# Optimization experiments

Measured on AMD Instinct MI355X. Metric: run time of the kernel, lower is better.

The kernel has to match this reference:

```python
import jax, jax.numpy as jnp
import numpy as np


def setup_inputs() -> dict:
    key = jax.random.key(0)
    k1, k2 = jax.random.split(key)
    n_tokens, embed_dim, num_embed = 16384, 512, 2048
    encode = jax.random.normal(k1, (n_tokens, embed_dim), dtype=jnp.float32)
    # Embedding init in torch: uniform(-1/num_embed, 1/num_embed)
    templat = jax.random.uniform(
        k2, (num_embed, embed_dim), dtype=jnp.float32,
        minval=-1.0 / num_embed, maxval=1.0 / num_embed)
    return {"encode": encode, "templat": templat}


def reference(encode, templat):
    # match_encode_with_templat, eval path: sample=False, detach='encode', metric='l2'
    encode_d = jax.lax.stop_gradient(encode)
    # squared L2 distance: ||e||^2 - 2 e@t^T + ||t||^2 ; logits = -dist
    e_sq = jnp.sum(encode_d * encode_d, axis=-1, keepdims=True)       # (N, 1)
    t_sq = jnp.sum(templat * templat, axis=-1)[None, :]               # (1, M)
    dist = e_sq - 2.0 * (encode_d @ templat.T) + t_sq                 # (N, M)
    logits = -dist
    zsoft = jax.nn.softmax(logits, axis=-1)
    zidx = jnp.argmax(zsoft, axis=-1)                                 # (N,)
    quant = templat[zidx]                                             # (N, C) gather
    return quant, zidx
```

## Files before the change

kernel.cpp:

```cpp
#include <hip/hip_runtime.h>
#include <stdint.h>

#define N_TOK  16384
#define EMB    512
#define NEMB   2048
#define NCHUNK 32
#define CWIN   2.5e-4f
#define WCAP   524288

typedef __attribute__((ext_vector_type(8))) short s16x8;
typedef __attribute__((ext_vector_type(4))) float f32x4;

__device__ __forceinline__ unsigned short f2bf(float f) {
  unsigned u = __float_as_uint(f);
  u += 0x7fffu + ((u >> 16) & 1u);
  return (unsigned short)(u >> 16);
}
__device__ __forceinline__ unsigned mapf(float f) {
  unsigned u = __float_as_uint(f);
  return (u >> 31) ? ~u : (u | 0x80000000u);
}
__device__ __forceinline__ float unmapf(unsigned u) {
  return __uint_as_float((u >> 31) ? (u & 0x7fffffffu) : ~u);
}

__device__ __forceinline__ float pairwise512_sq(const float* se, int lane) {
  int l = lane & 31;
  int b = l >> 3, j = l & 7;
  const float* base = se + b * 128 + j;
  float x = base[0];
  float r = __fmul_rn(x, x);
#pragma unroll
  for (int k = 1; k < 16; ++k) {
    float y = base[8 * k];
    r = __fadd_rn(r, __fmul_rn(y, y));
  }
  r = __fadd_rn(r, __shfl_xor(r, 1));
  r = __fadd_rn(r, __shfl_xor(r, 2));
  r = __fadd_rn(r, __shfl_xor(r, 4));
  r = __fadd_rn(r, __shfl_xor(r, 8));
  r = __fadd_rn(r, __shfl_xor(r, 16));
  return r;
}

__global__ __launch_bounds__(256) void prep_kernel(
    const float* __restrict__ tmp, const float* __restrict__ enc,
    unsigned short* __restrict__ thi, float* __restrict__ tsq,
    unsigned short* __restrict__ ehi, float* __restrict__ esq,
    int* __restrict__ wcount) {
  __shared__ float se[4][EMB];
  int wv = threadIdx.x >> 6, lane = threadIdx.x & 63;
  int row = blockIdx.x * 4 + wv;
  if (blockIdx.x == 0 && threadIdx.x == 0) *wcount = 0;
  bool isT = row < NEMB;
  const float* src = isT ? (tmp + (size_t)row * EMB)
                         : (enc + (size_t)(row - NEMB) * EMB);
  const float4* p = (const float4*)src + lane * 2;
  float4 v0 = p[0], v1 = p[1];
  float f[8] = {v0.x, v0.y, v0.z, v0.w, v1.x, v1.y, v1.z, v1.w};
  unsigned h[8];
#pragma unroll
  for (int i = 0; i < 8; ++i) { h[i] = f2bf(f[i]); se[wv][lane * 8 + i] = f[i]; }
  uint4 packed = { h[0] | (h[1] << 16), h[2] | (h[3] << 16),
                   h[4] | (h[5] << 16), h[6] | (h[7] << 16) };
  unsigned short* dsth = isT ? (thi + (size_t)row * EMB)
                             : (ehi + (size_t)(row - NEMB) * EMB);
  ((uint4*)dsth)[lane] = packed;
  __syncthreads();
  float s = pairwise512_sq(se[wv], lane);
  if (lane == 0) { if (isT) tsq[row] = s; else esq[row - NEMB] = s; }
}

__global__ __launch_bounds__(512, 2) void score_kernel(
    const unsigned short* __restrict__ ehi, const unsigned short* __restrict__ thi,
    const float* __restrict__ tsq,
    unsigned long long* __restrict__ keyc, unsigned* __restrict__ s2c) {
  __shared__ __align__(16) char smem[131072];
  const int tid = threadIdx.x, w = tid >> 6, lane = tid & 63;
  const int q = lane >> 4, r = lane & 15;
  const int wr = w >> 2, wc = w & 3;
  const int tokb = (int)blockIdx.x >> 3;
  const int nb   = (int)blockIdx.x & 7;

  const int c0 = tid, c1 = 512 + tid;
  const int L0 = (c0 * 16) ^ ((((c0 * 16) >> 9) & 1) << 5);
  const int L1 = (c1 * 16) ^ ((((c1 * 16) >> 9) & 1) << 5);
  const int row0 = L0 >> 6, ce0 = (L0 & 63) >> 1;
  const int row1 = L1 >> 6, ce1 = (L1 & 63) >> 1;
  const unsigned short* pa0 = ehi + (size_t)(tokb * 256 + row0) * EMB + ce0;
  const unsigned short* pa1 = ehi + (size_t)(tokb * 256 + row1) * EMB + ce1;
  const unsigned short* pb0 = thi + (size_t)(nb  * 256 + row0) * EMB + ce0;
  const unsigned short* pb1 = thi + (size_t)(nb  * 256 + row1) * EMB + ce1;

#define STAGE_A(ktp, kk) do {                                                     \
    char* lb_ = smem + ((((ktp) & 1) * 2 + (kk)) << 14) + (w << 10);              \
    __builtin_amdgcn_global_load_lds(                                             \
        (const __attribute__((address_space(1))) void*)(pa0 + (ktp) * 64 + (kk) * 32), \
        (__attribute__((address_space(3))) void*)lb_, 16, 0, 0);                  \
    __builtin_amdgcn_global_load_lds(                                             \
        (const __attribute__((address_space(1))) void*)(pa1 + (ktp) * 64 + (kk) * 32), \
        (__attribute__((address_space(3))) void*)(lb_ + 8192), 16, 0, 0);         \
  } while (0)
#define STAGE_B(ktp, kk) do {                                                     \
    char* lb_ = smem + 65536 + ((((ktp) & 1) * 2 + (kk)) << 14) + (w << 10);      \
    __builtin_amdgcn_global_load_lds(                                             \
        (const __attribute__((address_space(1))) void*)(pb0 + (ktp) * 64 + (kk) * 32), \
        (__attribute__((address_space(3))) void*)lb_, 16, 0, 0);                  \
    __builtin_amdgcn_global_load_lds(                                             \
        (const __attribute__((address_space(1))) void*)(pb1 + (ktp) * 64 + (kk) * 32), \
        (__attribute__((address_space(3))) void*)(lb_ + 8192), 16, 0, 0);         \
  } while (0)

  int offA[8], offB[4];
#pragma unroll
  for (int m = 0; m < 8; ++m) {
    int P = (wr * 128 + m * 16 + r) * 64 + q * 16;
    offA[m] = P ^ (((P >> 9) & 1) << 5);
  }
#pragma unroll
  for (int n = 0; n < 4; ++n) {
    int P = (wc * 64 + n * 16 + r) * 64 + q * 16;
    offB[n] = P ^ (((P >> 9) & 1) << 5);
  }

  f32x4 acc[8][4];
#pragma unroll
  for (int m = 0; m < 8; ++m)
#pragma unroll
    for (int n = 0; n < 4; ++n) acc[m][n] = (f32x4){0.f, 0.f, 0.f, 0.f};

  STAGE_A(0, 0); STAGE_B(0, 0); STAGE_A(0, 1); STAGE_B(0, 1); STAGE_A(1, 0); STAGE_B(1, 0);
  asm volatile("s_waitcnt vmcnt(8)" ::: "memory");
  __builtin_amdgcn_s_barrier();

#define LOADA(kkbase, mh)                                        \
    a0 = *(const s16x8*)(Ab_ + (kkbase) + offA[(mh) * 4 + 0]);   \
    a1 = *(const s16x8*)(Ab_ + (kkbase) + offA[(mh) * 4 + 1]);   \
    a2 = *(const s16x8*)(Ab_ + (kkbase) + offA[(mh) * 4 + 2]);   \
    a3 = *(const s16x8*)(Ab_ + (kkbase) + offA[(mh) * 4 + 3]);
#define LOADB(kkbase)                                            \
    bf4[0] = *(const s16x8*)(Bb_ + (kkbase) + offB[0]);          \
    bf4[1] = *(const s16x8*)(Bb_ + (kkbase) + offB[1]);          \
    bf4[2] = *(const s16x8*)(Bb_ + (kkbase) + offB[2]);          \
    bf4[3] = *(const s16x8*)(Bb_ + (kkbase) + offB[3]);
#define MFMA_HALF(mh)                                                              \
    __builtin_amdgcn_s_setprio(1);                                                 \
    _Pragma("unroll")                                                              \
    for (int n = 0; n < 4; ++n) {                                                  \
      acc[(mh) * 4 + 0][n] = __builtin_amdgcn_mfma_f32_16x16x32_bf16(a0, bf4[n], acc[(mh) * 4 + 0][n], 0, 0, 0); \
      acc[(mh) * 4 + 1][n] = __builtin_amdgcn_mfma_f32_16x16x32_bf16(a1, bf4[n], acc[(mh) * 4 + 1][n], 0, 0, 0); \
      acc[(mh) * 4 + 2][n] = __builtin_amdgcn_mfma_f32_16x16x32_bf16(a2, bf4[n], acc[(mh) * 4 + 2][n], 0, 0, 0); \
      acc[(mh) * 4 + 3][n] = __builtin_amdgcn_mfma_f32_16x16x32_bf16(a3, bf4[n], acc[(mh) * 4 + 3][n], 0, 0, 0); \
    }                                                                              \
    __builtin_amdgcn_s_setprio(0);

#pragma unroll
  for (int kt = 0; kt < 8; ++kt) {
    char* Ab_ = smem + ((kt & 1) * 2 << 14);
    char* Bb_ = smem + 65536 + ((kt & 1) * 2 << 14);
    s16x8 a0, a1, a2, a3, bf4[4];
    LOADA(0, 0); LOADB(0);
    if (kt + 1 < 8) STAGE_A(kt + 1, 1);
    __builtin_amdgcn_s_barrier();
    MFMA_HALF(0);
    __builtin_amdgcn_s_barrier();
    LOADA(0, 1);
    if (kt + 1 < 8) STAGE_B(kt + 1, 1);
    __builtin_amdgcn_s_barrier();
    MFMA_HALF(1);
    if (kt < 7) { asm volatile("s_waitcnt vmcnt(8)" ::: "memory"); }
    else        { asm volatile("s_waitcnt vmcnt(0)" ::: "memory"); }
    __builtin_amdgcn_s_barrier();
    LOADA(16384, 0); LOADB(16384);
    if (kt + 2 < 8) STAGE_A(kt + 2, 0);
    __builtin_amdgcn_s_barrier();
    MFMA_HALF(0);
    __builtin_amdgcn_s_barrier();
    LOADA(16384, 1);
    if (kt + 2 < 8) STAGE_B(kt + 2, 0);
    __builtin_amdgcn_s_barrier();
    MFMA_HALF(1);
    if (kt < 6)       { asm volatile("s_waitcnt vmcnt(8)" ::: "memory"); }
    else if (kt == 6) { asm volatile("s_waitcnt vmcnt(4)" ::: "memory"); }
    __builtin_amdgcn_s_barrier();
  }

  const int chunk = nb * 4 + wc;
  const int nbase = nb * 256 + wc * 64;
  float tq[4];
#pragma unroll
  for (int n = 0; n < 4; ++n) tq[n] = tsq[nbase + n * 16 + r];
#pragma unroll
  for (int m = 0; m < 8; ++m) {
#pragma unroll
    for (int i = 0; i < 4; ++i) {
      unsigned long long k1 = ~0ULL; unsigned s2m = 0xffffffffu;
#pragma unroll
      for (int n = 0; n < 4; ++n) {
        float s = tq[n] - 2.0f * acc[m][n][i];
        unsigned sm = mapf(s);
        unsigned long long k =
            ((unsigned long long)sm << 32) | (unsigned)(nbase + n * 16 + r);
        if (k < k1) { unsigned o = (unsigned)(k1 >> 32); s2m = o < s2m ? o : s2m; k1 = k; }
        else s2m = sm < s2m ? sm : s2m;
      }
#pragma unroll
      for (int mask = 1; mask < 16; mask <<= 1) {
        unsigned long long ok = __shfl_xor(k1, mask);
        unsigned os = __shfl_xor(s2m, mask);
        if (ok < k1) { unsigned o = (unsigned)(k1 >> 32); s2m = o < s2m ? o : s2m; k1 = ok; }
        else { unsigned o = (unsigned)(ok >> 32); s2m = o < s2m ? o : s2m; }
        s2m = os < s2m ? os : s2m;
      }
      if (r == 0) {
        int token = tokb * 256 + wr * 128 + m * 16 + q * 4 + i;
        keyc[(size_t)chunk * N_TOK + token] = k1;
        s2c [(size_t)chunk * N_TOK + token] = s2m;
      }
    }
  }
#undef STAGE_A
#undef STAGE_B
#undef LOADA
#undef LOADB
#undef MFMA_HALF
}

__global__ __launch_bounds__(64) void merge_kernel(
    const unsigned long long* __restrict__ keyc, const unsigned* __restrict__ s2c,
    int* __restrict__ bestIdx, int* __restrict__ flag, int* __restrict__ work,
    int* __restrict__ wcount, unsigned long long* __restrict__ rkey) {
  int t = blockIdx.x * 64 + threadIdx.x;
  if (t >= N_TOK) return;
  rkey[t] = ~0ULL;
  unsigned long long K = ~0ULL; unsigned S = 0xffffffffu;
  for (int c = 0; c < NCHUNK; ++c) {
    unsigned long long k = keyc[(size_t)c * N_TOK + t];
    unsigned s2 = s2c[(size_t)c * N_TOK + t];
    if (k < K) { unsigned o = (unsigned)(K >> 32); S = o < S ? o : S; K = k; }
    else { unsigned o = (unsigned)(k >> 32); S = o < S ? o : S; }
    S = s2 < S ? s2 : S;
  }
  float best_f   = unmapf((unsigned)(K >> 32));
  float second_f = unmapf(S);
  int idx = (int)(unsigned)(K & 0xffffffffu);
  bestIdx[t] = idx;
  bool ok = (second_f - best_f >= CWIN) && (idx >= 0) && (idx < NEMB) && (best_f == best_f);
  flag[t] = ok ? 0 : 1;
  if (!ok) {
    bool nanCase = !(best_f == best_f);
    float limit = best_f + CWIN;
    for (int c = 0; c < NCHUNK; ++c) {
      float cf = unmapf((unsigned)(keyc[(size_t)c * N_TOK + t] >> 32));
      if (nanCase || !(cf > limit)) {
        int pos = atomicAdd(wcount, 1);
        if (pos < WCAP) work[pos] = t * NCHUNK + c;
      }
    }
  }
}

__global__ __launch_bounds__(256) void refine_kernel(
    const float* __restrict__ enc, const float* __restrict__ tmp,
    const float* __restrict__ esq, const float* __restrict__ tsq,
    const int* __restrict__ work, const int* __restrict__ wcount,
    unsigned long long* __restrict__ rkey) {
  int total = *wcount; if (total > WCAP) total = WCAP;
  __shared__ float se[EMB];
  const int wv = threadIdx.x >> 6, lane = threadIdx.x & 63;
  for (int p = blockIdx.x; p < total; p += gridDim.x) {
    __syncthreads();
    int item = work[p];
    int token = item / NCHUNK, c = item % NCHUNK;
    const float4* erow = (const float4*)(enc + (size_t)token * EMB);
    for (int i = threadIdx.x; i < 128; i += 256) ((float4*)se)[i] = erow[i];
    __syncthreads();
    float e2 = esq[token];
    unsigned long long lkey = ~0ULL;
#pragma unroll
    for (int j = 0; j < 16; ++j) {
      int m = c * 64 + wv + j * 4;
      const float4* trow = (const float4*)(tmp + (size_t)m * EMB);
      float4 a0 = trow[lane], a1 = trow[lane + 64];
      float4 b0 = ((const float4*)se)[lane], b1 = ((const float4*)se)[lane + 64];
      double s = (double)a0.x * b0.x + (double)a0.y * b0.y
               + (double)a0.z * b0.z + (double)a0.w * b0.w
               + (double)a1.x * b1.x + (double)a1.y * b1.y
               + (double)a1.z * b1.z + (double)a1.w * b1.w;
#pragma unroll
      for (int mask = 1; mask < 64; mask <<= 1) s += __shfl_xor(s, mask);
      if (lane == 0) {
        float M  = (float)s;
        float d1 = __fadd_rn(e2, -__fmul_rn(2.0f, M));
        float d2 = __fadd_rn(d1, tsq[m]);
        unsigned long long key =
            ((unsigned long long)__float_as_uint(d2) << 32) | (unsigned)m;
        if (key < lkey) lkey = key;
      }
    }
    if (lane == 0 && lkey != ~0ULL) atomicMin(&rkey[token], lkey);
  }
}

__global__ void gather_kernel(const float* __restrict__ tmp, const int* __restrict__ bestIdx,
                              const int* __restrict__ flag,
                              const unsigned long long* __restrict__ rkey,
                              float* __restrict__ out) {
  int token = blockIdx.x * 4 + (threadIdx.x >> 6);
  int lane = threadIdx.x & 63;
  int idx = flag[token] ? (int)(unsigned)(rkey[token] & 0xffffffffULL) : bestIdx[token];
  idx = idx < 0 ? 0 : (idx > NEMB - 1 ? NEMB - 1 : idx);
  const float4* src = (const float4*)(tmp + (size_t)idx * EMB) + lane * 2;
  float4* dst = (float4*)(out + (size_t)token * EMB) + lane * 2;
  dst[0] = src[0];
  dst[1] = src[1];
  if (lane == 0) out[(size_t)N_TOK * EMB + token] = (float)idx;
}

extern "C" void kernel_launch(void* const* d_in, const int* in_sizes, int n_in,
                              void* d_out, int out_size, void* d_ws, size_t ws_size,
                              hipStream_t stream) {
  const float* enc = (const float*)d_in[0];
  const float* tmp = (const float*)d_in[1];
  float* out = (float*)d_out;
  char* ws = (char*)d_ws;
  unsigned short* thi = (unsigned short*)ws;
  unsigned short* ehi = (unsigned short*)(ws + 2097152);
  float* tsq      = (float*)(ws + 18874368);
  float* esq      = (float*)(ws + 18882560);
  unsigned long long* keyc = (unsigned long long*)(ws + 18948096);
  unsigned* s2c   = (unsigned*)(ws + 23142400);
  int*   bestIdx  = (int*)  (ws + 25239552);
  int*   flag     = (int*)  (ws + 25305088);
  unsigned long long* rkey = (unsigned long long*)(ws + 25370624);
  int*   wcount   = (int*)  (ws + 25501696);
  int*   work     = (int*)  (ws + 25501760);

  prep_kernel  <<<4608,      256, 0, stream>>>(tmp, enc, thi, tsq, ehi, esq, wcount);
  score_kernel <<<512,       512, 0, stream>>>(ehi, thi, tsq, keyc, s2c);
  merge_kernel <<<N_TOK/64,  64,  0, stream>>>(keyc, s2c, bestIdx, flag, work, wcount, rkey);
  refine_kernel<<<1024,      256, 0, stream>>>(enc, tmp, esq, tsq, work, wcount, rkey);
  gather_kernel<<<N_TOK/4,   256, 0, stream>>>(tmp, bestIdx, flag, rkey, out);
}
```

Baseline: 209.3 us.

## Process two codebook tiles per score block and use DPP reductions in epilogue

Each score block now computes two 256-wide codebook tiles in sequence and reuses its token tile. The grid drops to 256 blocks with a swizzled block-to-tile mapping, and the next tile's loads are issued before the current epilogue runs. The epilogue's 64-bit key shuffle reduction is replaced by float min and second-min folding over DPP lane swaps, followed by an index recovery pass and vectorized stores. The refine kernel gives each 16-lane group one codebook row instead of having a whole wave reduce over 64 lanes, and the merge kernel uses larger blocks. Running half as many blocks may lower occupancy and CU coverage on a 256-CU device.

```diff
diff --git a/kernel.cpp b/kernel.cpp
--- a/kernel.cpp
+++ b/kernel.cpp
@@ -22,6 +22,16 @@
 }
 __device__ __forceinline__ float unmapf(unsigned u) {
   return __uint_as_float((u >> 31) ? (u & 0x7fffffffu) : ~u);
+}
+
+template<int CTRL>
+__device__ __forceinline__ float dppf(float x) {
+  return __uint_as_float((unsigned)__builtin_amdgcn_update_dpp(
+      0, (int)__float_as_uint(x), CTRL, 0xF, 0xF, true));
+}
+template<int CTRL>
+__device__ __forceinline__ unsigned dppu(unsigned x) {
+  return (unsigned)__builtin_amdgcn_update_dpp(0, (int)x, CTRL, 0xF, 0xF, true);
 }
 
 __device__ __forceinline__ float pairwise512_sq(const float* se, int lane) {
@@ -79,8 +89,10 @@
   const int tid = threadIdx.x, w = tid >> 6, lane = tid & 63;
   const int q = lane >> 4, r = lane & 15;
   const int wr = w >> 2, wc = w & 3;
-  const int tokb = (int)blockIdx.x >> 3;
-  const int nb   = (int)blockIdx.x & 7;
+  const int bid = (int)blockIdx.x;
+  const int sw = (bid & 7) * 32 + (bid >> 3);
+  const int tokb = sw >> 2;
+  const int nbq  = sw & 3;
 
   const int c0 = tid, c1 = 512 + tid;
   const int L0 = (c0 * 16) ^ ((((c0 * 16) >> 9) & 1) << 5);
@@ -89,8 +101,8 @@
   const int row1 = L1 >> 6, ce1 = (L1 & 63) >> 1;
   const unsigned short* pa0 = ehi + (size_t)(tokb * 256 + row0) * EMB + ce0;
   const unsigned short* pa1 = ehi + (size_t)(tokb * 256 + row1) * EMB + ce1;
-  const unsigned short* pb0 = thi + (size_t)(nb  * 256 + row0) * EMB + ce0;
-  const unsigned short* pb1 = thi + (size_t)(nb  * 256 + row1) * EMB + ce1;
+  const unsigned short* pb0 = thi + (size_t)(nbq * 512 + row0) * EMB + ce0;
+  const unsigned short* pb1 = thi + (size_t)(nbq * 512 + row1) * EMB + ce1;
 
 #define STAGE_A(ktp, kk) do {                                                     \
     char* lb_ = smem + ((((ktp) & 1) * 2 + (kk)) << 14) + (w << 10);              \
@@ -122,16 +134,6 @@
     int P = (wc * 64 + n * 16 + r) * 64 + q * 16;
     offB[n] = P ^ (((P >> 9) & 1) << 5);
   }
-
-  f32x4 acc[8][4];
-#pragma unroll
-  for (int m = 0; m < 8; ++m)
-#pragma unroll
-    for (int n = 0; n < 4; ++n) acc[m][n] = (f32x4){0.f, 0.f, 0.f, 0.f};
-
-  STAGE_A(0, 0); STAGE_B(0, 0); STAGE_A(0, 1); STAGE_B(0, 1); STAGE_A(1, 0); STAGE_B(1, 0);
-  asm volatile("s_waitcnt vmcnt(8)" ::: "memory");
-  __builtin_amdgcn_s_barrier();
 
 #define LOADA(kkbase, mh)                                        \
     a0 = *(const s16x8*)(Ab_ + (kkbase) + offA[(mh) * 4 + 0]);   \
@@ -154,69 +156,100 @@
     }                                                                              \
     __builtin_amdgcn_s_setprio(0);
 
-#pragma unroll
-  for (int kt = 0; kt < 8; ++kt) {
-    char* Ab_ = smem + ((kt & 1) * 2 << 14);
-    char* Bb_ = smem + 65536 + ((kt & 1) * 2 << 14);
-    s16x8 a0, a1, a2, a3, bf4[4];
-    LOADA(0, 0); LOADB(0);
-    if (kt + 1 < 8) STAGE_A(kt + 1, 1);
+  f32x4 acc[8][4];
+
+  STAGE_A(0, 0); STAGE_B(0, 0); STAGE_A(0, 1); STAGE_B(0, 1); STAGE_A(1, 0); STAGE_B(1, 0);
+
+#pragma unroll 1
+  for (int half = 0; half < 2; ++half) {
+    if (half == 0) { asm volatile("s_waitcnt vmcnt(8)" ::: "memory"); }
+    else           { asm volatile("s_waitcnt vmcnt(0)" ::: "memory"); }
     __builtin_amdgcn_s_barrier();
-    MFMA_HALF(0);
-    __builtin_amdgcn_s_barrier();
-    LOADA(0, 1);
-    if (kt + 1 < 8) STAGE_B(kt + 1, 1);
-    __builtin_amdgcn_s_barrier();
-    MFMA_HALF(1);
-    if (kt < 7) { asm volatile("s_waitcnt vmcnt(8)" ::: "memory"); }
-    else        { asm volatile("s_waitcnt vmcnt(0)" ::: "memory"); }
-    __builtin_amdgcn_s_barrier();
-    LOADA(16384, 0); LOADB(16384);
-    if (kt + 2 < 8) STAGE_A(kt + 2, 0);
-    __builtin_amdgcn_s_barrier();
-    MFMA_HALF(0);
-    __builtin_amdgcn_s_barrier();
-    LOADA(16384, 1);
-    if (kt + 2 < 8) STAGE_B(kt + 2, 0);
-    __builtin_amdgcn_s_barrier();
-    MFMA_HALF(1);
-    if (kt < 6)       { asm volatile("s_waitcnt vmcnt(8)" ::: "memory"); }
-    else if (kt == 6) { asm volatile("s_waitcnt vmcnt(4)" ::: "memory"); }
-    __builtin_amdgcn_s_barrier();
-  }
-
-  const int chunk = nb * 4 + wc;
-  const int nbase = nb * 256 + wc * 64;
-  float tq[4];
-#pragma unroll
-  for (int n = 0; n < 4; ++n) tq[n] = tsq[nbase + n * 16 + r];
-#pragma unroll
-  for (int m = 0; m < 8; ++m) {
-#pragma unroll
-    for (int i = 0; i < 4; ++i) {
-      unsigned long long k1 = ~0ULL; unsigned s2m = 0xffffffffu;
-#pragma unroll
-      for (int n = 0; n < 4; ++n) {
-        float s = tq[n] - 2.0f * acc[m][n][i];
-        unsigned sm = mapf(s);
-        unsigned long long k =
-            ((unsigned long long)sm << 32) | (unsigned)(nbase + n * 16 + r);
-        if (k < k1) { unsigned o = (unsigned)(k1 >> 32); s2m = o < s2m ? o : s2m; k1 = k; }
-        else s2m = sm < s2m ? sm : s2m;
+
+#pragma unroll
+    for (int ti = 0; ti < 8; ++ti)
+#pragma unroll
+      for (int j = 0; j < 4; ++j) acc[ti][j] = (f32x4){0.f, 0.f, 0.f, 0.f};
+
+#pragma unroll
+    for (int kt = 0; kt < 8; ++kt) {
+      char* Ab_ = smem + ((kt & 1) * 2 << 14);
+      char* Bb_ = smem + 65536 + ((kt & 1) * 2 << 14);
+      s16x8 a0, a1, a2, a3, bf4[4];
+      LOADA(0, 0); LOADB(0);
+      if (kt + 1 < 8) STAGE_A(kt + 1, 1);
+      __builtin_amdgcn_s_barrier();
+      MFMA_HALF(0);
+      __builtin_amdgcn_s_barrier();
+      LOADA(0, 1);
+      if (kt + 1 < 8) STAGE_B(kt + 1, 1);
+      __builtin_amdgcn_s_barrier();
+      MFMA_HALF(1);
+      if (kt < 7) { asm volatile("s_waitcnt vmcnt(8)" ::: "memory"); }
+      else        { asm volatile("s_waitcnt vmcnt(0)" ::: "memory"); }
+      __builtin_amdgcn_s_barrier();
+      LOADA(16384, 0); LOADB(16384);
+      if (kt + 2 < 8) STAGE_A(kt + 2, 0);
+      __builtin_amdgcn_s_barrier();
+      MFMA_HALF(0);
+      __builtin_amdgcn_s_barrier();
+      LOADA(16384, 1);
+      if (kt + 2 < 8) STAGE_B(kt + 2, 0);
+      __builtin_amdgcn_s_barrier();
+      MFMA_HALF(1);
+      if (kt < 6)       { asm volatile("s_waitcnt vmcnt(8)" ::: "memory"); }
+      else if (kt == 6) { asm volatile("s_waitcnt vmcnt(4)" ::: "memory"); }
+      __builtin_amdgcn_s_barrier();
+    }
+
+    if (half == 0) {
+      pb0 += (size_t)256 * EMB; pb1 += (size_t)256 * EMB;
+      STAGE_A(0, 0); STAGE_B(0, 0); STAGE_A(0, 1); STAGE_B(0, 1); STAGE_A(1, 0); STAGE_B(1, 0);
+    }
+
+    {
+      const int nb = nbq * 2 + half;
+      const int chunk = nb * 4 + wc;
+      const int nbase = nb * 256 + wc * 64;
+      const float tq0 = tsq[nbase + r], tq1 = tsq[nbase + 16 + r],
+                  tq2 = tsq[nbase + 32 + r], tq3 = tsq[nbase + 48 + r];
+#define FOLD(CTRL) { float os_ = dppf<CTRL>(sb), os2_ = dppf<CTRL>(s2f);        \
+      float mx_ = fmaxf(sb, os_);                                               \
+      s2f = fminf(fminf(s2f, os2_), mx_); sb = fminf(sb, os_); }
+#define FOLDL(CTRL) { unsigned ol_ = dppu<CTRL>(li); li = li < ol_ ? li : ol_; }
+#pragma unroll
+      for (int m = 0; m < 8; ++m) {
+        unsigned long long kk[4]; unsigned ss[4];
+#pragma unroll
+        for (int i = 0; i < 4; ++i) {
+          float s0 = fmaf(-2.f, acc[m][0][i], tq0);
+          float s1 = fmaf(-2.f, acc[m][1][i], tq1);
+          float s2v = fmaf(-2.f, acc[m][2][i], tq2);
+          float s3 = fmaf(-2.f, acc[m][3][i], tq3);
+          float n01 = fminf(s0, s1), X01 = fmaxf(s0, s1);
+          float n23 = fminf(s2v, s3), X23 = fmaxf(s2v, s3);
+          float sb = fminf(n01, n23);
+          float s2f = fminf(fminf(X01, X23), fmaxf(n01, n23));
+          FOLD(0xB1) FOLD(0x4E) FOLD(0x124) FOLD(0x128)
+          unsigned li = 0xFFFFFFFFu;
+          li = (s3  == sb) ? (unsigned)(48 + r) : li;
+          li = (s2v == sb) ? (unsigned)(32 + r) : li;
+          li = (s1  == sb) ? (unsigned)(16 + r) : li;
+          li = (s0  == sb) ? (unsigned)(r)      : li;
+          FOLDL(0xB1) FOLDL(0x4E) FOLDL(0x124) FOLDL(0x128)
+          kk[i] = ((unsigned long long)mapf(sb) << 32) | (unsigned)(nbase + (int)li);
+          ss[i] = mapf(s2f);
+        }
+        if (r == 0) {
+          size_t base = (size_t)chunk * N_TOK +
+                        (size_t)(tokb * 256 + wr * 128 + m * 16 + q * 4);
+          ((ulonglong2*)&keyc[base])[0] = make_ulonglong2(kk[0], kk[1]);
+          ((ulonglong2*)&keyc[base])[1] = make_ulonglong2(kk[2], kk[3]);
+          *(uint4*)&s2c[base] = make_uint4(ss[0], ss[1], ss[2], ss[3]);
+        }
       }
-#pragma unroll
-      for (int mask = 1; mask < 16; mask <<= 1) {
-        unsigned long long ok = __shfl_xor(k1, mask);
-        unsigned os = __shfl_xor(s2m, mask);
-        if (ok < k1) { unsigned o = (unsigned)(k1 >> 32); s2m = o < s2m ? o : s2m; k1 = ok; }
-        else { unsigned o = (unsigned)(ok >> 32); s2m = o < s2m ? o : s2m; }
-        s2m = os < s2m ? os : s2m;
-      }
-      if (r == 0) {
-        int token = tokb * 256 + wr * 128 + m * 16 + q * 4 + i;
-        keyc[(size_t)chunk * N_TOK + token] = k1;
-        s2c [(size_t)chunk * N_TOK + token] = s2m;
-      }
+#undef FOLD
+#undef FOLDL
     }
   }
 #undef STAGE_A
@@ -226,11 +259,11 @@
 #undef MFMA_HALF
 }
 
-__global__ __launch_bounds__(64) void merge_kernel(
+__global__ __launch_bounds__(256) void merge_kernel(
     const unsigned long long* __restrict__ keyc, const unsigned* __restrict__ s2c,
     int* __restrict__ bestIdx, int* __restrict__ flag, int* __restrict__ work,
     int* __restrict__ wcount, unsigned long long* __restrict__ rkey) {
-  int t = blockIdx.x * 64 + threadIdx.x;
+  int t = blockIdx.x * 256 + threadIdx.x;
   if (t >= N_TOK) return;
   rkey[t] = ~0ULL;
   unsigned long long K = ~0ULL; unsigned S = 0xffffffffu;
@@ -268,6 +301,7 @@
   int total = *wcount; if (total > WCAP) total = WCAP;
   __shared__ float se[EMB];
   const int wv = threadIdx.x >> 6, lane = threadIdx.x & 63;
+  const int g = lane >> 4, l16 = lane & 15;
   for (int p = blockIdx.x; p < total; p += gridDim.x) {
     __syncthreads();
     int item = work[p];
@@ -278,18 +312,20 @@
     float e2 = esq[token];
     unsigned long long lkey = ~0ULL;
 #pragma unroll
-    for (int j = 0; j < 16; ++j) {
-      int m = c * 64 + wv + j * 4;
+    for (int j = 0; j < 4; ++j) {
+      int m = c * 64 + wv * 16 + j * 4 + g;
       const float4* trow = (const float4*)(tmp + (size_t)m * EMB);
-      float4 a0 = trow[lane], a1 = trow[lane + 64];
-      float4 b0 = ((const float4*)se)[lane], b1 = ((const float4*)se)[lane + 64];
-      double s = (double)a0.x * b0.x + (double)a0.y * b0.y
-               + (double)a0.z * b0.z + (double)a0.w * b0.w
-               + (double)a1.x * b1.x + (double)a1.y * b1.y
-               + (double)a1.z * b1.z + (double)a1.w * b1.w;
-#pragma unroll
-      for (int mask = 1; mask < 64; mask <<= 1) s += __shfl_xor(s, mask);
-      if (lane == 0) {
+      double s = 0.0;
+#pragma unroll
+      for (int k = 0; k < 8; ++k) {
+        float4 a = trow[l16 + 16 * k];
+        float4 b = ((const float4*)se)[l16 + 16 * k];
+        s += (double)a.x * b.x + (double)a.y * b.y
+           + (double)a.z * b.z + (double)a.w * b.w;
+      }
+      s += __shfl_xor(s, 1); s += __shfl_xor(s, 2);
+      s += __shfl_xor(s, 4); s += __shfl_xor(s, 8);
+      if (l16 == 0) {
         float M  = (float)s;
         float d1 = __fadd_rn(e2, -__fmul_rn(2.0f, M));
         float d2 = __fadd_rn(d1, tsq[m]);
@@ -298,7 +334,7 @@
         if (key < lkey) lkey = key;
       }
     }
-    if (lane == 0 && lkey != ~0ULL) atomicMin(&rkey[token], lkey);
+    if (l16 == 0 && lkey != ~0ULL) atomicMin(&rkey[token], lkey);
   }
 }
 
@@ -337,8 +373,8 @@
   int*   work     = (int*)  (ws + 25501760);
 
   prep_kernel  <<<4608,      256, 0, stream>>>(tmp, enc, thi, tsq, ehi, esq, wcount);
-  score_kernel <<<512,       512, 0, stream>>>(ehi, thi, tsq, keyc, s2c);
-  merge_kernel <<<N_TOK/64,  64,  0, stream>>>(keyc, s2c, bestIdx, flag, work, wcount, rkey);
+  score_kernel <<<256,       512, 0, stream>>>(ehi, thi, tsq, keyc, s2c);
+  merge_kernel <<<N_TOK/256, 256, 0, stream>>>(keyc, s2c, bestIdx, flag, work, wcount, rkey);
   refine_kernel<<<1024,      256, 0, stream>>>(enc, tmp, esq, tsq, work, wcount, rkey);
   gather_kernel<<<N_TOK/4,   256, 0, stream>>>(tmp, bestIdx, flag, rkey, out);
 }
```

Result: faster. 205.0 us (-2.1%).

## Remap score block order, widen merge blocks, split refine dot products across 16-lane groups

Applied to the files above, without the earlier changes.

Three separate changes. The score kernel's block-to-tile mapping is permuted so that blocks placed on the same XCD (bid & 7) share token tiles, which should improve L2 reuse of the encode and template tiles. The merge kernel uses 256-thread blocks instead of 64. The refine kernel now computes four template dot products per wavefront at once, one per 16-lane group, so each needs only four shuffle steps instead of six, at the cost of uneven lane utilisation in the loads.

```diff
diff --git a/kernel.cpp b/kernel.cpp
--- a/kernel.cpp
+++ b/kernel.cpp
@@ -79,8 +79,13 @@
   const int tid = threadIdx.x, w = tid >> 6, lane = tid & 63;
   const int q = lane >> 4, r = lane & 15;
   const int wr = w >> 2, wc = w & 3;
-  const int tokb = (int)blockIdx.x >> 3;
-  const int nb   = (int)blockIdx.x & 7;
+  const int bid = (int)blockIdx.x;
+  const int x   = bid & 7;
+  const int j   = bid >> 3;
+  const int rho = j >> 5;
+  const int cc  = j & 31;
+  const int tokb = x * 8 + rho * 4 + (cc >> 3);
+  const int nb   = cc & 7;
 
   const int c0 = tid, c1 = 512 + tid;
   const int L0 = (c0 * 16) ^ ((((c0 * 16) >> 9) & 1) << 5);
@@ -226,11 +231,11 @@
 #undef MFMA_HALF
 }
 
-__global__ __launch_bounds__(64) void merge_kernel(
+__global__ __launch_bounds__(256) void merge_kernel(
     const unsigned long long* __restrict__ keyc, const unsigned* __restrict__ s2c,
     int* __restrict__ bestIdx, int* __restrict__ flag, int* __restrict__ work,
     int* __restrict__ wcount, unsigned long long* __restrict__ rkey) {
-  int t = blockIdx.x * 64 + threadIdx.x;
+  int t = blockIdx.x * 256 + threadIdx.x;
   if (t >= N_TOK) return;
   rkey[t] = ~0ULL;
   unsigned long long K = ~0ULL; unsigned S = 0xffffffffu;
@@ -268,6 +273,7 @@
   int total = *wcount; if (total > WCAP) total = WCAP;
   __shared__ float se[EMB];
   const int wv = threadIdx.x >> 6, lane = threadIdx.x & 63;
+  const int g = lane >> 4, l16 = lane & 15;
   for (int p = blockIdx.x; p < total; p += gridDim.x) {
     __syncthreads();
     int item = work[p];
@@ -278,18 +284,20 @@
     float e2 = esq[token];
     unsigned long long lkey = ~0ULL;
 #pragma unroll
-    for (int j = 0; j < 16; ++j) {
-      int m = c * 64 + wv + j * 4;
+    for (int j = 0; j < 4; ++j) {
+      int m = c * 64 + wv * 16 + j * 4 + g;
       const float4* trow = (const float4*)(tmp + (size_t)m * EMB);
-      float4 a0 = trow[lane], a1 = trow[lane + 64];
-      float4 b0 = ((const float4*)se)[lane], b1 = ((const float4*)se)[lane + 64];
-      double s = (double)a0.x * b0.x + (double)a0.y * b0.y
-               + (double)a0.z * b0.z + (double)a0.w * b0.w
-               + (double)a1.x * b1.x + (double)a1.y * b1.y
-               + (double)a1.z * b1.z + (double)a1.w * b1.w;
-#pragma unroll
-      for (int mask = 1; mask < 64; mask <<= 1) s += __shfl_xor(s, mask);
-      if (lane == 0) {
+      double s = 0.0;
+#pragma unroll
+      for (int k = 0; k < 8; ++k) {
+        float4 a = trow[l16 + 16 * k];
+        float4 b = ((const float4*)se)[l16 + 16 * k];
+        s += (double)a.x * b.x + (double)a.y * b.y
+           + (double)a.z * b.z + (double)a.w * b.w;
+      }
+      s += __shfl_xor(s, 1); s += __shfl_xor(s, 2);
+      s += __shfl_xor(s, 4); s += __shfl_xor(s, 8);
+      if (l16 == 0) {
         float M  = (float)s;
         float d1 = __fadd_rn(e2, -__fmul_rn(2.0f, M));
         float d2 = __fadd_rn(d1, tsq[m]);
@@ -298,7 +306,7 @@
         if (key < lkey) lkey = key;
       }
     }
-    if (lane == 0 && lkey != ~0ULL) atomicMin(&rkey[token], lkey);
+    if (l16 == 0 && lkey != ~0ULL) atomicMin(&rkey[token], lkey);
   }
 }
 
@@ -338,7 +346,7 @@
 
   prep_kernel  <<<4608,      256, 0, stream>>>(tmp, enc, thi, tsq, ehi, esq, wcount);
   score_kernel <<<512,       512, 0, stream>>>(ehi, thi, tsq, keyc, s2c);
-  merge_kernel <<<N_TOK/64,  64,  0, stream>>>(keyc, s2c, bestIdx, flag, work, wcount, rkey);
+  merge_kernel <<<N_TOK/256, 256, 0, stream>>>(keyc, s2c, bestIdx, flag, work, wcount, rkey);
   refine_kernel<<<1024,      256, 0, stream>>>(enc, tmp, esq, tsq, work, wcount, rkey);
   gather_kernel<<<N_TOK/4,   256, 0, stream>>>(tmp, bestIdx, flag, rkey, out);
 }
```

New measurement: 188.8 us. -9.8%, faster.
